# Kernel tuning notes

Hardware: AMD Instinct MI355X
Metric: run time of the kernel (lower is better)

## Reference

```python
import jax, jax.numpy as jnp
import numpy as np

# 24 unique dyadic offsets (powers of 2 and 3*2^k), max < N
UNIQUE_OFFSETS = np.array([0, 1, 2, 3, 4, 6, 8, 12, 16, 24, 32, 48, 64, 96, 128,
                           192, 256, 384, 512, 768, 1024, 1536, 2048, 3072], dtype=np.int32)
B, N, D, H = 1, 4096, 1024, 16
HD = D // H


def setup_inputs() -> dict:
    key = jax.random.key(0)
    ks = jax.random.split(key, 8)
    s = D ** -0.5
    return {
        "x": jax.random.normal(ks[0], (B, N, D), jnp.float32),
        "Wqkv": jax.random.normal(ks[1], (D, 3 * D), jnp.float32) * s,
        "bqkv": jnp.zeros((3 * D,), jnp.float32),
        "Wout": jax.random.normal(ks[2], (D, D), jnp.float32) * s,
        "bout": jnp.zeros((D,), jnp.float32),
        "Wgate": jax.random.normal(ks[3], (D, D), jnp.float32) * s,
        "bgate": jnp.full((D,), 2.0, jnp.float32),  # nn.init.constant_(gate_proj.bias, 2.0)
        "pos_bias": jax.random.normal(ks[4], (len(UNIQUE_OFFSETS), H), jnp.float32) * 0.1,
    }


def reference(x, Wqkv, bqkv, Wout, bout, Wgate, bgate, pos_bias):
    b, n, d = x.shape
    scale = HD ** -0.5
    qkv = x @ Wqkv + bqkv                       # [B,N,3D]
    q, k, v = jnp.split(qkv, 3, axis=-1)
    def heads(t):
        return t.reshape(b, n, H, HD).transpose(0, 2, 1, 3)  # [B,H,N,HD]
    q, k, v = heads(q), heads(k), heads(v)

    deltas = jnp.asarray(UNIQUE_OFFSETS)        # [O]
    idx = jnp.arange(n)[:, None] - deltas[None, :]   # [N,O] source position t-delta
    valid = (idx >= 0).astype(x.dtype)[:, :, None]   # [N,O,1]; covers delta>=N too
    idxc = jnp.clip(idx, 0, n - 1)

    k_g = k[:, :, idxc, :] * valid              # [B,H,N,O,HD] gathered, zero-padded
    v_g = v[:, :, idxc, :] * valid

    # score_{t,i} = q_t . k_{t-delta_i} * scale + pos_bias[i, head]
    scores = jnp.einsum('bhnd,bhnod->bhno', q, k_g) * scale + pos_bias.T[None, :, None, :]
    attn = jax.nn.softmax(scores, axis=-1)      # softmax over 24 taps
    out = jnp.einsum('bhno,bhnod->bhnd', attn, v_g)

    out_flat = out.transpose(0, 2, 1, 3).reshape(b, n, d)
    gate = jax.nn.sigmoid(x @ Wgate + bgate)
    return (out_flat * gate) @ Wout + bout      # dropout is identity in eval
```

## Files before the change

kernel.cpp:

```cpp
#include <hip/hip_runtime.h>
#include <hip/hip_bf16.h>

#define NN 4096
#define DD 1024
#define HH 16
#define HDD 64
#define NO 24
#define QKV_N (3 * DD)

typedef short bf16x8 __attribute__((ext_vector_type(8)));
typedef float f32x4 __attribute__((ext_vector_type(4)));
typedef unsigned short ushort;

__device__ __forceinline__ ushort f2bf(float f) {
    unsigned u = __float_as_uint(f);
    return (ushort)((u + 0x7FFFu + ((u >> 16) & 1u)) >> 16);
}
__device__ __forceinline__ float bf2f(ushort u) {
    return __uint_as_float(((unsigned)u) << 16);
}

__device__ __forceinline__ void gload16(const void* g, void* l) {
    __builtin_amdgcn_global_load_lds((const __attribute__((address_space(1))) void*)g,
                                     (__attribute__((address_space(3))) void*)l, 16, 0, 0);
}

__device__ __forceinline__ int tap_delta(int j) {
    return j < 2 ? j : (2 + (j & 1)) << ((j >> 1) - 1);
}

__global__ __launch_bounds__(256) void f2b_kernel(const float* __restrict__ in,
                                                  ushort* __restrict__ out, int n4) {
    int i = blockIdx.x * 256 + threadIdx.x;
    if (i < n4) {
        float4 v = ((const float4*)in)[i];
        ushort4 o;
        o.x = f2bf(v.x); o.y = f2bf(v.y); o.z = f2bf(v.z); o.w = f2bf(v.w);
        ((ushort4*)out)[i] = o;
    }
}

__global__ __launch_bounds__(256) void transpose_f2b(const float* __restrict__ in,
                                                     ushort* __restrict__ out,
                                                     int R, int C) {
    __shared__ float tile[32][33];
    const int c0 = blockIdx.x * 32, r0 = blockIdx.y * 32;
    const int tx = threadIdx.x & 31, ty = threadIdx.x >> 5;
#pragma unroll
    for (int i = 0; i < 32; i += 8)
        tile[ty + i][tx] = in[(size_t)(r0 + ty + i) * C + c0 + tx];
    __syncthreads();
#pragma unroll
    for (int i = 0; i < 32; i += 8)
        out[(size_t)(c0 + ty + i) * R + r0 + tx] = f2bf(tile[tx][ty + i]);
}

template <int OP>
__global__ __launch_bounds__(256) void mfma_gemm(const ushort* __restrict__ A,
                                                 const ushort* __restrict__ BT,
                                                 const float* __restrict__ bias,
                                                 const void* __restrict__ mult,
                                                 void* __restrict__ Cout,
                                                 int M, int N, int K) {
    __shared__ ushort sA[2][128 * 32];
    __shared__ ushort sB[2][128 * 32];

    const int tid = threadIdx.x;
    const int lane = tid & 63;
    const int w = tid >> 6;
    const int wr = w >> 1, wc = w & 1;
    const int m0 = blockIdx.y * 128, n0 = blockIdx.x * 128;

    const int row0 = tid >> 2, slot = tid & 3;
    const int row1 = row0 + 64;
    const int sw0 = slot ^ ((row0 >> 1) & 3);
    const int sw1 = slot ^ ((row1 >> 1) & 3);
    const int dst0 = (tid & ~63) * 8;
    const int dst1 = (256 + (tid & ~63)) * 8;

    const size_t aOff0 = (size_t)(m0 + row0) * K + sw0 * 8;
    const size_t aOff1 = (size_t)(m0 + row1) * K + sw1 * 8;
    const size_t bOff0 = (size_t)(n0 + row0) * K + sw0 * 8;
    const size_t bOff1 = (size_t)(n0 + row1) * K + sw1 * 8;

    const int ks = lane >> 4;
    int aRd[4], bRd[4];
#pragma unroll
    for (int m = 0; m < 4; ++m) {
        int r = wr * 64 + m * 16 + (lane & 15);
        aRd[m] = r * 64 + ((ks ^ ((r >> 1) & 3)) << 4);
    }
#pragma unroll
    for (int n = 0; n < 4; ++n) {
        int r = wc * 64 + n * 16 + (lane & 15);
        bRd[n] = r * 64 + ((ks ^ ((r >> 1) & 3)) << 4);
    }

    f32x4 acc[4][4];
#pragma unroll
    for (int m = 0; m < 4; ++m)
#pragma unroll
        for (int n = 0; n < 4; ++n) acc[m][n] = (f32x4){0.f, 0.f, 0.f, 0.f};

#define STAGE(buf, k0)                                              \
    do {                                                            \
        gload16(A + aOff0 + (k0), &sA[buf][dst0]);                  \
        gload16(A + aOff1 + (k0), &sA[buf][dst1]);                  \
        gload16(BT + bOff0 + (k0), &sB[buf][dst0]);                 \
        gload16(BT + bOff1 + (k0), &sB[buf][dst1]);                 \
    } while (0)

    const int NS = K >> 5;
    STAGE(0, 0);
    for (int s = 0; s < NS; ++s) {
        const int cur = s & 1;
        __syncthreads();
        if (s + 1 < NS) STAGE(cur ^ 1, (s + 1) * 32);
        const char* pa = (const char*)sA[cur];
        const char* pb = (const char*)sB[cur];
        bf16x8 af[4], bfr[4];
#pragma unroll
        for (int m = 0; m < 4; ++m) af[m] = *(const bf16x8*)(pa + aRd[m]);
#pragma unroll
        for (int n = 0; n < 4; ++n) bfr[n] = *(const bf16x8*)(pb + bRd[n]);
#pragma unroll
        for (int m = 0; m < 4; ++m)
#pragma unroll
            for (int n = 0; n < 4; ++n)
                acc[m][n] = __builtin_amdgcn_mfma_f32_16x16x32_bf16(af[m], bfr[n],
                                                                    acc[m][n], 0, 0, 0);
    }
#undef STAGE

    const int fr = lane & 15, fq = lane >> 4;
#pragma unroll
    for (int m = 0; m < 4; ++m) {
        const int rbase = m0 + wr * 64 + m * 16 + fq * 4;
#pragma unroll
        for (int n = 0; n < 4; ++n) {
            const int col = n0 + wc * 64 + n * 16 + fr;
            const float bv = bias[col];
#pragma unroll
            for (int j = 0; j < 4; ++j) {
                float v = acc[m][n][j] + bv;
                if (OP == 0) {
                    ((float*)Cout)[(size_t)(rbase + j) * N + col] = v;
                } else if (OP == 1) {
                    ((ushort*)Cout)[(size_t)(rbase + j) * N + col] = f2bf(v);
                } else {
                    const float mu =
                        bf2f(((const ushort*)mult)[(size_t)(rbase + j) * N + col]);
                    v = mu / (1.f + expf(-v));
                    ((ushort*)Cout)[(size_t)(rbase + j) * N + col] = f2bf(v);
                }
            }
        }
    }
}

__global__ __launch_bounds__(256) void attn_kernel(const ushort* __restrict__ qkv,
                                                   const float* __restrict__ pos_bias,
                                                   ushort* __restrict__ outp) {
    const int bid = (blockIdx.x & 7) * 2048 + (blockIdx.x >> 3);
    const int w = threadIdx.x >> 6;
    const int lane = threadIdx.x & 63;
    const int g = lane >> 3;
    const int e = lane & 7;
    const int h = bid >> 10;
    const int t = (bid & 1023) * 4 + w;

    const int d0 = h * HDD + e * 8;

    bf16x8 q8 = *(const bf16x8*)(qkv + (size_t)t * QKV_N + d0);
    float qf[8];
#pragma unroll
    for (int i = 0; i < 8; ++i) qf[i] = bf2f((ushort)q8[i]);

    float sc[3];
    float pv_p[3];
    int rowz[3];
    bool valid[3];
#pragma unroll
    for (int r = 0; r < 3; ++r) {
        const int j = 8 * r + g;
        const int dlt = tap_delta(j);
        valid[r] = (t >= dlt);
        rowz[r] = valid[r] ? (t - dlt) : 0;
        bf16x8 k8 = *(const bf16x8*)(qkv + (size_t)rowz[r] * QKV_N + DD + d0);
        float dot = 0.f;
#pragma unroll
        for (int i = 0; i < 8; ++i) dot = fmaf(qf[i], bf2f((ushort)k8[i]), dot);
        dot += __shfl_xor(dot, 1);
        dot += __shfl_xor(dot, 2);
        dot += __shfl_xor(dot, 4);
        const float pb = pos_bias[j * HH + h];
        sc[r] = valid[r] ? fmaf(dot, 0.125f, pb) : pb;
    }

    float mx = fmaxf(fmaxf(sc[0], sc[1]), sc[2]);
    mx = fmaxf(mx, __shfl_xor(mx, 8));
    mx = fmaxf(mx, __shfl_xor(mx, 16));
    mx = fmaxf(mx, __shfl_xor(mx, 32));
    float ex[3];
#pragma unroll
    for (int r = 0; r < 3; ++r) ex[r] = __expf(sc[r] - mx);
    float den = ex[0] + ex[1] + ex[2];
    den += __shfl_xor(den, 8);
    den += __shfl_xor(den, 16);
    den += __shfl_xor(den, 32);
    const float inv = 1.f / den;
#pragma unroll
    for (int r = 0; r < 3; ++r) pv_p[r] = valid[r] ? ex[r] * inv : 0.f;

    float o[8];
#pragma unroll
    for (int i = 0; i < 8; ++i) o[i] = 0.f;
#pragma unroll
    for (int r = 0; r < 3; ++r) {
        bf16x8 v8 = *(const bf16x8*)(qkv + (size_t)rowz[r] * QKV_N + 2 * DD + d0);
#pragma unroll
        for (int i = 0; i < 8; ++i) o[i] = fmaf(pv_p[r], bf2f((ushort)v8[i]), o[i]);
    }
#pragma unroll
    for (int i = 0; i < 8; ++i) {
        o[i] += __shfl_xor(o[i], 8);
        o[i] += __shfl_xor(o[i], 16);
        o[i] += __shfl_xor(o[i], 32);
    }

    if (g == 0) {
        bf16x8 o8;
#pragma unroll
        for (int i = 0; i < 8; ++i) o8[i] = (short)f2bf(o[i]);
        *(bf16x8*)(outp + (size_t)t * DD + d0) = o8;
    }
}

extern "C" void kernel_launch(void* const* d_in, const int* in_sizes, int n_in,
                              void* d_out, int out_size, void* d_ws, size_t ws_size,
                              hipStream_t stream) {
    const float* x = (const float*)d_in[0];
    const float* Wqkv = (const float*)d_in[1];
    const float* bqkv = (const float*)d_in[2];
    const float* Wout = (const float*)d_in[3];
    const float* bout = (const float*)d_in[4];
    const float* Wgate = (const float*)d_in[5];
    const float* bgate = (const float*)d_in[6];
    const float* pos_bias = (const float*)d_in[7];
    float* out = (float*)d_out;

    char* ws = (char*)d_ws;
    ushort* xb = (ushort*)ws;
    ushort* WqkvT = (ushort*)(ws + ((size_t)8 << 20));
    ushort* WgateT = (ushort*)(ws + ((size_t)14 << 20));
    ushort* WoutT = (ushort*)(ws + ((size_t)16 << 20));
    ushort* qkv = (ushort*)(ws + ((size_t)18 << 20));
    ushort* attno = (ushort*)(ws + ((size_t)42 << 20));
    ushort* gated = (ushort*)(ws + ((size_t)50 << 20));

    f2b_kernel<<<(NN * DD / 4 + 255) / 256, 256, 0, stream>>>(x, xb, NN * DD / 4);
    transpose_f2b<<<dim3(QKV_N / 32, DD / 32), 256, 0, stream>>>(Wqkv, WqkvT, DD, QKV_N);
    transpose_f2b<<<dim3(DD / 32, DD / 32), 256, 0, stream>>>(Wgate, WgateT, DD, DD);
    transpose_f2b<<<dim3(DD / 32, DD / 32), 256, 0, stream>>>(Wout, WoutT, DD, DD);

    mfma_gemm<1><<<dim3(QKV_N / 128, NN / 128), 256, 0, stream>>>(
        xb, WqkvT, bqkv, nullptr, qkv, NN, QKV_N, DD);
    attn_kernel<<<16384, 256, 0, stream>>>(qkv, pos_bias, attno);
    mfma_gemm<2><<<dim3(DD / 128, NN / 128), 256, 0, stream>>>(
        xb, WgateT, bgate, attno, gated, NN, DD, DD);
    mfma_gemm<0><<<dim3(DD / 128, NN / 128), 256, 0, stream>>>(
        gated, WoutT, bout, nullptr, out, NN, DD, DD);
}
```

Baseline: 211.9 us.

## Fuse gate projection into QKV GEMM and apply gating in attention

Concatenates the transposed Wgate after Wqkv so a single GEMM over N=4096 produces q, k, v and the sigmoid gate, with the sigmoid applied in the epilogue for columns past 3*D. The attention kernel then loads the gate values and multiplies them into its output before writing bf16, so the separate gate GEMM launch and its read of the attention output are removed. The cost is a wider QKV GEMM output buffer and an extra per-thread gate load in attention. The weight layout requires WcatT to occupy 8 MB, which fits exactly before WoutT at the 16 MB offset.

```diff
diff --git a/kernel.cpp b/kernel.cpp
--- a/kernel.cpp
+++ b/kernel.cpp
@@ -6,7 +6,7 @@
 #define HH 16
 #define HDD 64
 #define NO 24
-#define QKV_N (3 * DD)
+#define QG_N 4096
 
 typedef short bf16x8 __attribute__((ext_vector_type(8)));
 typedef float f32x4 __attribute__((ext_vector_type(4)));
@@ -58,8 +58,9 @@
 template <int OP>
 __global__ __launch_bounds__(256) void mfma_gemm(const ushort* __restrict__ A,
                                                  const ushort* __restrict__ BT,
-                                                 const float* __restrict__ bias,
-                                                 const void* __restrict__ mult,
+                                                 const float* __restrict__ bias0,
+                                                 const float* __restrict__ bias1,
+                                                 int sigStart,
                                                  void* __restrict__ Cout,
                                                  int M, int N, int K) {
     __shared__ ushort sA[2][128 * 32];
@@ -139,18 +140,15 @@
 #pragma unroll
         for (int n = 0; n < 4; ++n) {
             const int col = n0 + wc * 64 + n * 16 + fr;
-            const float bv = bias[col];
+            const bool sig = (col >= sigStart);
+            const float bv = sig ? bias1[col - sigStart] : bias0[col];
 #pragma unroll
             for (int j = 0; j < 4; ++j) {
                 float v = acc[m][n][j] + bv;
+                if (sig) v = 1.f / (1.f + expf(-v));
                 if (OP == 0) {
                     ((float*)Cout)[(size_t)(rbase + j) * N + col] = v;
-                } else if (OP == 1) {
-                    ((ushort*)Cout)[(size_t)(rbase + j) * N + col] = f2bf(v);
                 } else {
-                    const float mu =
-                        bf2f(((const ushort*)mult)[(size_t)(rbase + j) * N + col]);
-                    v = mu / (1.f + expf(-v));
                     ((ushort*)Cout)[(size_t)(rbase + j) * N + col] = f2bf(v);
                 }
             }
@@ -158,7 +156,7 @@
     }
 }
 
-__global__ __launch_bounds__(256) void attn_kernel(const ushort* __restrict__ qkv,
+__global__ __launch_bounds__(256) void attn_kernel(const ushort* __restrict__ qkvg,
                                                    const float* __restrict__ pos_bias,
                                                    ushort* __restrict__ outp) {
     const int bid = (blockIdx.x & 7) * 2048 + (blockIdx.x >> 3);
@@ -171,7 +169,7 @@
 
     const int d0 = h * HDD + e * 8;
 
-    bf16x8 q8 = *(const bf16x8*)(qkv + (size_t)t * QKV_N + d0);
+    bf16x8 q8 = *(const bf16x8*)(qkvg + (size_t)t * QG_N + d0);
     float qf[8];
 #pragma unroll
     for (int i = 0; i < 8; ++i) qf[i] = bf2f((ushort)q8[i]);
@@ -186,7 +184,7 @@
         const int dlt = tap_delta(j);
         valid[r] = (t >= dlt);
         rowz[r] = valid[r] ? (t - dlt) : 0;
-        bf16x8 k8 = *(const bf16x8*)(qkv + (size_t)rowz[r] * QKV_N + DD + d0);
+        bf16x8 k8 = *(const bf16x8*)(qkvg + (size_t)rowz[r] * QG_N + DD + d0);
         float dot = 0.f;
 #pragma unroll
         for (int i = 0; i < 8; ++i) dot = fmaf(qf[i], bf2f((ushort)k8[i]), dot);
@@ -217,7 +215,7 @@
     for (int i = 0; i < 8; ++i) o[i] = 0.f;
 #pragma unroll
     for (int r = 0; r < 3; ++r) {
-        bf16x8 v8 = *(const bf16x8*)(qkv + (size_t)rowz[r] * QKV_N + 2 * DD + d0);
+        bf16x8 v8 = *(const bf16x8*)(qkvg + (size_t)rowz[r] * QG_N + 2 * DD + d0);
 #pragma unroll
         for (int i = 0; i < 8; ++i) o[i] = fmaf(pv_p[r], bf2f((ushort)v8[i]), o[i]);
     }
@@ -229,9 +227,11 @@
     }
 
     if (g == 0) {
+        bf16x8 g8 = *(const bf16x8*)(qkvg + (size_t)t * QG_N + 3 * DD + d0);
         bf16x8 o8;
 #pragma unroll
-        for (int i = 0; i < 8; ++i) o8[i] = (short)f2bf(o[i]);
+        for (int i = 0; i < 8; ++i)
+            o8[i] = (short)f2bf(o[i] * bf2f((ushort)g8[i]));
         *(bf16x8*)(outp + (size_t)t * DD + d0) = o8;
     }
 }
@@ -251,23 +251,20 @@
 
     char* ws = (char*)d_ws;
     ushort* xb = (ushort*)ws;
-    ushort* WqkvT = (ushort*)(ws + ((size_t)8 << 20));
-    ushort* WgateT = (ushort*)(ws + ((size_t)14 << 20));
+    ushort* WcatT = (ushort*)(ws + ((size_t)8 << 20));
     ushort* WoutT = (ushort*)(ws + ((size_t)16 << 20));
-    ushort* qkv = (ushort*)(ws + ((size_t)18 << 20));
-    ushort* attno = (ushort*)(ws + ((size_t)42 << 20));
+    ushort* qkvg = (ushort*)(ws + ((size_t)18 << 20));
     ushort* gated = (ushort*)(ws + ((size_t)50 << 20));
 
     f2b_kernel<<<(NN * DD / 4 + 255) / 256, 256, 0, stream>>>(x, xb, NN * DD / 4);
-    transpose_f2b<<<dim3(QKV_N / 32, DD / 32), 256, 0, stream>>>(Wqkv, WqkvT, DD, QKV_N);
-    transpose_f2b<<<dim3(DD / 32, DD / 32), 256, 0, stream>>>(Wgate, WgateT, DD, DD);
+    transpose_f2b<<<dim3(3 * DD / 32, DD / 32), 256, 0, stream>>>(Wqkv, WcatT, DD, 3 * DD);
+    transpose_f2b<<<dim3(DD / 32, DD / 32), 256, 0, stream>>>(
+        Wgate, WcatT + (size_t)3 * DD * DD, DD, DD);
     transpose_f2b<<<dim3(DD / 32, DD / 32), 256, 0, stream>>>(Wout, WoutT, DD, DD);
 
-    mfma_gemm<1><<<dim3(QKV_N / 128, NN / 128), 256, 0, stream>>>(
-        xb, WqkvT, bqkv, nullptr, qkv, NN, QKV_N, DD);
-    attn_kernel<<<16384, 256, 0, stream>>>(qkv, pos_bias, attno);
-    mfma_gemm<2><<<dim3(DD / 128, NN / 128), 256, 0, stream>>>(
-        xb, WgateT, bgate, attno, gated, NN, DD, DD);
+    mfma_gemm<1><<<dim3(QG_N / 128, NN / 128), 256, 0, stream>>>(
+        xb, WcatT, bqkv, bgate, 3 * DD, qkvg, NN, QG_N, DD);
+    attn_kernel<<<16384, 256, 0, stream>>>(qkvg, pos_bias, gated);
     mfma_gemm<0><<<dim3(DD / 128, NN / 128), 256, 0, stream>>>(
-        gated, WoutT, bout, nullptr, out, NN, DD, DD);
-}
+        gated, WoutT, bout, bout, 1 << 30, out, NN, DD, DD);
+}
```

After: 207.0 us. -2.3%, faster.
